# Kernel tuning notes

Hardware: AMD Instinct MI355X
Metric: run time of the kernel (lower is better)

The kernel has to match this reference:

```python
import jax, jax.numpy as jnp
import numpy as np

E = 1_000_000   # total edges across batch
B = 1024        # n_batch (graphs)
IN = 128
OUT = 128


def setup_inputs() -> dict:
    key = jax.random.key(0)
    ks = jax.random.split(key, 8)
    x1 = jax.random.normal(ks[0], (E, IN), dtype=jnp.float32)
    # cumulative slice boundaries: [0, sorted interior cuts, E]
    inner = jnp.sort(jax.random.randint(ks[1], (B - 1,), 0, E))
    edge_slices = jnp.concatenate([jnp.zeros((1,), jnp.int32),
                                   inner.astype(jnp.int32),
                                   jnp.full((1,), E, jnp.int32)])
    s1 = 1.0 / np.sqrt(IN)
    s2 = 1.0 / np.sqrt(OUT)
    W1 = jax.random.uniform(ks[2], (IN, OUT), jnp.float32, -s1, s1)
    b1 = jax.random.uniform(ks[3], (OUT,), jnp.float32, -s1, s1)
    W2 = jax.random.uniform(ks[4], (OUT, OUT), jnp.float32, -s2, s2)
    b2 = jax.random.uniform(ks[5], (OUT,), jnp.float32, -s2, s2)
    W3 = jax.random.uniform(ks[6], (OUT, OUT), jnp.float32, -s2, s2)
    b3 = jax.random.uniform(ks[7], (OUT,), jnp.float32, -s2, s2)
    return {"x1": x1, "edge_slices": edge_slices,
            "W1": W1, "b1": b1, "W2": W2, "b2": b2, "W3": W3, "b3": b3}


def reference(x1, edge_slices, W1, b1, W2, b2, W3, b3):
    n_edges = x1.shape[0]
    n_batch = edge_slices.shape[0] - 1
    # internal MLP: Linear -> ReLU -> Linear
    h = jax.nn.relu(x1 @ W1 + b1) @ W2 + b2  # [E, OUT]
    # segment id of edge i: index of slice containing i (replaces repeat_interleave)
    seg = jnp.searchsorted(edge_slices[1:], jnp.arange(n_edges), side='right')
    sums = jax.ops.segment_sum(h, seg, num_segments=n_batch)        # [B, OUT]
    counts = (edge_slices[1:] - edge_slices[:-1]).astype(h.dtype)   # [B]
    mean = sums / jnp.maximum(counts, 1.0)[:, None]  # empty segments -> 0 (matches scatter-mean)
    # external MLP: single Linear
    return mean @ W3 + b3
```

## Files before the change

### kernel.cpp

```cpp
#include <hip/hip_runtime.h>
#include <hip/hip_bf16.h>

typedef __attribute__((ext_vector_type(8))) short short8;
typedef __attribute__((ext_vector_type(4))) float floatx4;
typedef unsigned short u16;
typedef unsigned int u32;

#define D 128
#define TM 64
#define NT 4
#define CHUNK (TM*NT)
#define LDSX 136

static __device__ __forceinline__ u16 f2bf(float f) {
  union { float f; u32 u; } v; v.f = f;
  u32 r = v.u + 0x7fffu + ((v.u >> 16) & 1u);
  return (u16)(r >> 16);
}

__global__ void prep_kernel(const float* __restrict__ W1, u16* __restrict__ W1T,
                            float* __restrict__ S, int nS)
{
  int t = blockIdx.x * blockDim.x + threadIdx.x;
  if (t < D * D) {
    int k = t >> 7;
    int n = t & (D - 1);
    W1T[n * D + k] = f2bf(W1[t]);
  }
  if (t < nS) S[t] = 0.f;
}

__global__ __launch_bounds__(256, 3)
void fused_mlp_segsum(const float* __restrict__ x1,
                      const int* __restrict__ slices,
                      const u16* __restrict__ W1T,
                      const float* __restrict__ b1,
                      float* __restrict__ S,
                      int E, int B)
{
  __shared__ __align__(16) u16 xt[2][TM * LDSX];

  const int tid  = threadIdx.x;
  const int wv   = tid >> 6;
  const int lane = tid & 63;
  const int quad = lane >> 4;
  const int l16  = lane & 15;

  const int chunkStart = blockIdx.x * CHUNK;
  const int chunkEnd   = min(chunkStart + CHUNK, E);
  const int ntiles     = (chunkEnd - chunkStart + TM - 1) / TM;

  short8 bf[2][4];
  #pragma unroll
  for (int c = 0; c < 2; ++c)
    #pragma unroll
    for (int kk = 0; kk < 4; ++kk)
      bf[c][kk] = *(const short8*)(W1T + ((2 * wv + c) * 16 + l16) * D + kk * 32 + quad * 8);

  float bias[2] = { b1[wv * 32 + l16], b1[wv * 32 + 16 + l16] };

  int l = 0, r = B + 1;
  while (l < r) { int m = (l + r) >> 1; if (slices[m] <= chunkStart) l = m + 1; else r = m; }
  int cur = l - 1;
  float racc0 = 0.f, racc1 = 0.f;

  {
    #pragma unroll
    for (int i = 0; i < 8; ++i) {
      int f = tid + i * 256;
      int row = chunkStart + (f >> 5);
      int c = (f & 31) * 4;
      int rr = min(row, E - 1);
      float4 v = *(const float4*)(x1 + (size_t)rr * D + c);
      if (row >= E) { v.x = 0.f; v.y = 0.f; v.z = 0.f; v.w = 0.f; }
      uint2 pk;
      pk.x = (u32)f2bf(v.x) | ((u32)f2bf(v.y) << 16);
      pk.y = (u32)f2bf(v.z) | ((u32)f2bf(v.w) << 16);
      *(uint2*)(&xt[0][(f >> 5) * LDSX + c]) = pk;
    }
  }
  __syncthreads();

  for (int t = 0; t < ntiles; ++t) {
    const int base = chunkStart + t * TM;

    float4 ld[8];
    const bool havePf = (t + 1 < ntiles);
    if (havePf) {
      int nb = base + TM;
      #pragma unroll
      for (int i = 0; i < 8; ++i) {
        int f = tid + i * 256;
        int row = nb + (f >> 5);
        int rr = min(row, E - 1);
        ld[i] = *(const float4*)(x1 + (size_t)rr * D + (f & 31) * 4);
        if (row >= E) { ld[i].x = 0.f; ld[i].y = 0.f; ld[i].z = 0.f; ld[i].w = 0.f; }
      }
    }

    const u16* xb = xt[t & 1];
    floatx4 acc[4][2];
    #pragma unroll
    for (int rt = 0; rt < 4; ++rt)
      #pragma unroll
      for (int c = 0; c < 2; ++c)
        acc[rt][c] = (floatx4){0.f, 0.f, 0.f, 0.f};

    #pragma unroll
    for (int kk = 0; kk < 4; ++kk) {
      #pragma unroll
      for (int rt = 0; rt < 4; ++rt) {
        short8 a = *(const short8*)(xb + (rt * 16 + l16) * LDSX + kk * 32 + quad * 8);
        acc[rt][0] = __builtin_amdgcn_mfma_f32_16x16x32_bf16(a, bf[0][kk], acc[rt][0], 0, 0, 0);
        acc[rt][1] = __builtin_amdgcn_mfma_f32_16x16x32_bf16(a, bf[1][kk], acc[rt][1], 0, 0, 0);
      }
    }

    #pragma unroll
    for (int rt = 0; rt < 4; ++rt)
      #pragma unroll
      for (int c = 0; c < 2; ++c)
        #pragma unroll
        for (int i = 0; i < 4; ++i)
          acc[rt][c][i] = fmaxf(acc[rt][c][i] + bias[c], 0.f);

    const int tileHi = min(base + TM, chunkEnd);

    auto segAdd = [&](int loR, int hiR) {
      #pragma unroll
      for (int rt = 0; rt < 4; ++rt)
        #pragma unroll
        for (int i = 0; i < 4; ++i) {
          int rowOff = rt * 16 + quad * 4 + i;
          bool in = (rowOff >= loR) && (rowOff < hiR);
          racc0 += in ? acc[rt][0][i] : 0.f;
          racc1 += in ? acc[rt][1][i] : 0.f;
        }
    };
    auto flushSeg = [&](int s) {
      float t0 = racc0, t1 = racc1;
      t0 += __shfl_xor(t0, 16); t0 += __shfl_xor(t0, 32);
      t1 += __shfl_xor(t1, 16); t1 += __shfl_xor(t1, 32);
      if (quad == 0) {
        atomicAdd(&S[s * D + wv * 32 + l16], t0);
        atomicAdd(&S[s * D + wv * 32 + 16 + l16], t1);
      }
    };

    while (cur < B) {
      int segEnd = slices[cur + 1];
      if (segEnd > tileHi) break;
      int lo = max(slices[cur], base);
      if (segEnd > lo) segAdd(lo - base, segEnd - base);
      flushSeg(cur);
      racc0 = 0.f; racc1 = 0.f;
      ++cur;
    }
    if (cur < B) {
      int lo = max(slices[cur], base);
      if (lo < tileHi) {
        if (lo == base && tileHi == base + TM) {
          #pragma unroll
          for (int rt = 0; rt < 4; ++rt)
            #pragma unroll
            for (int i = 0; i < 4; ++i) { racc0 += acc[rt][0][i]; racc1 += acc[rt][1][i]; }
        } else {
          segAdd(lo - base, tileHi - base);
        }
      }
    }

    if (havePf) {
      u16* dst = xt[(t + 1) & 1];
      #pragma unroll
      for (int i = 0; i < 8; ++i) {
        int f = tid + i * 256;
        uint2 pk;
        pk.x = (u32)f2bf(ld[i].x) | ((u32)f2bf(ld[i].y) << 16);
        pk.y = (u32)f2bf(ld[i].z) | ((u32)f2bf(ld[i].w) << 16);
        *(uint2*)(&dst[(f >> 5) * LDSX + (f & 31) * 4]) = pk;
      }
    }
    __syncthreads();
  }

  if (cur < B && slices[cur] < chunkEnd) {
    float t0 = racc0, t1 = racc1;
    t0 += __shfl_xor(t0, 16); t0 += __shfl_xor(t0, 32);
    t1 += __shfl_xor(t1, 16); t1 += __shfl_xor(t1, 32);
    if (quad == 0) {
      atomicAdd(&S[cur * D + wv * 32 + l16], t0);
      atomicAdd(&S[cur * D + wv * 32 + 16 + l16], t1);
    }
  }
}

__global__ __launch_bounds__(128)
void finish_mlp(const float* __restrict__ S, const int* __restrict__ slices,
                const float* __restrict__ W2, const float* __restrict__ b2,
                const float* __restrict__ W3, const float* __restrict__ b3,
                float* __restrict__ out, int B)
{
  __shared__ float v0[D];
  __shared__ float v1[D];
  int s = blockIdx.x;
  int j = threadIdx.x;
  int c0 = slices[s], c1 = slices[s + 1];
  int cnt = c1 - c0;
  if (cnt <= 0) { out[s * D + j] = b3[j]; return; }
  v0[j] = S[s * D + j] * (1.f / (float)cnt);
  __syncthreads();
  float a = b2[j];
  #pragma unroll 8
  for (int k = 0; k < D; ++k) a = fmaf(v0[k], W2[k * D + j], a);
  v1[j] = a;
  __syncthreads();
  float o = b3[j];
  #pragma unroll 8
  for (int k = 0; k < D; ++k) o = fmaf(v1[k], W3[k * D + j], o);
  out[s * D + j] = o;
}

extern "C" void kernel_launch(void* const* d_in, const int* in_sizes, int n_in,
                              void* d_out, int out_size, void* d_ws, size_t ws_size,
                              hipStream_t stream) {
  const float* x1     = (const float*)d_in[0];
  const int*   slices = (const int*)d_in[1];
  const float* W1     = (const float*)d_in[2];
  const float* b1     = (const float*)d_in[3];
  const float* W2     = (const float*)d_in[4];
  const float* b2     = (const float*)d_in[5];
  const float* W3     = (const float*)d_in[6];
  const float* b3     = (const float*)d_in[7];
  float* out = (float*)d_out;

  const int E = in_sizes[0] / D;
  const int B = in_sizes[1] - 1;

  float* S   = (float*)d_ws;
  u16*   W1T = (u16*)((char*)d_ws + (size_t)B * D * 4);

  int nS = B * D;
  prep_kernel<<<(nS + 255) / 256, 256, 0, stream>>>(W1, W1T, S, nS);

  int nblk = (E + CHUNK - 1) / CHUNK;
  fused_mlp_segsum<<<nblk, 256, 0, stream>>>(x1, slices, W1T, b1, S, E, B);

  finish_mlp<<<B, D, 0, stream>>>(S, slices, W2, b2, W3, b3, out, B);
}
```

Before: 675.8 us.

## Stage x1 tiles into LDS via direct global-to-LDS loads with swizzle

```diff
diff --git a/kernel.cpp b/kernel.cpp
--- a/kernel.cpp
+++ b/kernel.cpp
@@ -7,16 +7,23 @@
 typedef unsigned int u32;
 
 #define D 128
-#define TM 64
-#define NT 4
+#define TM 32
+#define NT 8
 #define CHUNK (TM*NT)
-#define LDSX 136
 
 static __device__ __forceinline__ u16 f2bf(float f) {
   union { float f; u32 u; } v; v.f = f;
   u32 r = v.u + 0x7fffu + ((v.u >> 16) & 1u);
   return (u16)(r >> 16);
 }
+
+static __device__ __forceinline__ u32 pk2(float x, float y) {
+  union { __hip_bfloat162 h; u32 u; } c;
+  c.h = __float22bfloat162_rn(make_float2(x, y));
+  return c.u;
+}
+
+union S8u { short8 s; u32 u[4]; };
 
 __global__ void prep_kernel(const float* __restrict__ W1, u16* __restrict__ W1T,
                             float* __restrict__ S, int nS)
@@ -30,7 +37,7 @@
   if (t < nS) S[t] = 0.f;
 }
 
-__global__ __launch_bounds__(256, 3)
+__global__ __launch_bounds__(256, 4)
 void fused_mlp_segsum(const float* __restrict__ x1,
                       const int* __restrict__ slices,
                       const u16* __restrict__ W1T,
@@ -38,7 +45,7 @@
                       float* __restrict__ S,
                       int E, int B)
 {
-  __shared__ __align__(16) u16 xt[2][TM * LDSX];
+  __shared__ __align__(16) float xt[2][TM * D];
 
   const int tid  = threadIdx.x;
   const int wv   = tid >> 6;
@@ -59,49 +66,45 @@
 
   float bias[2] = { b1[wv * 32 + l16], b1[wv * 32 + 16 + l16] };
 
+  const int idxA = l16 * D + ((( quad * 2     ) ^ (l16 & 7)) << 2);
+  const int idxB = l16 * D + (((quad * 2 + 1) ^ (l16 & 7)) << 2);
+
+  const int pg  = lane & 31;
+  const int rhi = lane >> 5;
+
+  auto stage = [&](float* buf, int rowBase) {
+    #pragma unroll
+    for (int i = 0; i < 4; ++i) {
+      int rs = wv * 8 + i * 2 + rhi;
+      int lg = (pg & 24) | ((pg ^ rs) & 7);
+      int grow = min(rowBase + rs, E - 1);
+      const float* src = x1 + (size_t)grow * D + lg * 4;
+      float* dst = buf + rs * D + pg * 4;
+      __builtin_amdgcn_global_load_lds(
+          (const __attribute__((address_space(1))) void*)src,
+          (__attribute__((address_space(3))) void*)dst, 16, 0, 0);
+    }
+  };
+
   int l = 0, r = B + 1;
   while (l < r) { int m = (l + r) >> 1; if (slices[m] <= chunkStart) l = m + 1; else r = m; }
   int cur = l - 1;
+  int curStart = slices[cur];
+  int nextEnd  = slices[cur + 1];
   float racc0 = 0.f, racc1 = 0.f;
 
-  {
-    #pragma unroll
-    for (int i = 0; i < 8; ++i) {
-      int f = tid + i * 256;
-      int row = chunkStart + (f >> 5);
-      int c = (f & 31) * 4;
-      int rr = min(row, E - 1);
-      float4 v = *(const float4*)(x1 + (size_t)rr * D + c);
-      if (row >= E) { v.x = 0.f; v.y = 0.f; v.z = 0.f; v.w = 0.f; }
-      uint2 pk;
-      pk.x = (u32)f2bf(v.x) | ((u32)f2bf(v.y) << 16);
-      pk.y = (u32)f2bf(v.z) | ((u32)f2bf(v.w) << 16);
-      *(uint2*)(&xt[0][(f >> 5) * LDSX + c]) = pk;
-    }
-  }
+  stage(xt[0], chunkStart);
   __syncthreads();
 
   for (int t = 0; t < ntiles; ++t) {
     const int base = chunkStart + t * TM;
 
-    float4 ld[8];
-    const bool havePf = (t + 1 < ntiles);
-    if (havePf) {
-      int nb = base + TM;
-      #pragma unroll
-      for (int i = 0; i < 8; ++i) {
-        int f = tid + i * 256;
-        int row = nb + (f >> 5);
-        int rr = min(row, E - 1);
-        ld[i] = *(const float4*)(x1 + (size_t)rr * D + (f & 31) * 4);
-        if (row >= E) { ld[i].x = 0.f; ld[i].y = 0.f; ld[i].z = 0.f; ld[i].w = 0.f; }
-      }
-    }
-
-    const u16* xb = xt[t & 1];
-    floatx4 acc[4][2];
-    #pragma unroll
-    for (int rt = 0; rt < 4; ++rt)
+    if (t + 1 < ntiles) stage(xt[(t + 1) & 1], base + TM);
+
+    const float* xb = xt[t & 1];
+    floatx4 acc[2][2];
+    #pragma unroll
+    for (int rt = 0; rt < 2; ++rt)
       #pragma unroll
       for (int c = 0; c < 2; ++c)
         acc[rt][c] = (floatx4){0.f, 0.f, 0.f, 0.f};
@@ -109,15 +112,19 @@
     #pragma unroll
     for (int kk = 0; kk < 4; ++kk) {
       #pragma unroll
-      for (int rt = 0; rt < 4; ++rt) {
-        short8 a = *(const short8*)(xb + (rt * 16 + l16) * LDSX + kk * 32 + quad * 8);
-        acc[rt][0] = __builtin_amdgcn_mfma_f32_16x16x32_bf16(a, bf[0][kk], acc[rt][0], 0, 0, 0);
-        acc[rt][1] = __builtin_amdgcn_mfma_f32_16x16x32_bf16(a, bf[1][kk], acc[rt][1], 0, 0, 0);
+      for (int rt = 0; rt < 2; ++rt) {
+        float4 fa = *(const float4*)(xb + idxA + rt * 2048 + kk * 32);
+        float4 fb = *(const float4*)(xb + idxB + rt * 2048 + kk * 32);
+        S8u a;
+        a.u[0] = pk2(fa.x, fa.y); a.u[1] = pk2(fa.z, fa.w);
+        a.u[2] = pk2(fb.x, fb.y); a.u[3] = pk2(fb.z, fb.w);
+        acc[rt][0] = __builtin_amdgcn_mfma_f32_16x16x32_bf16(a.s, bf[0][kk], acc[rt][0], 0, 0, 0);
+        acc[rt][1] = __builtin_amdgcn_mfma_f32_16x16x32_bf16(a.s, bf[1][kk], acc[rt][1], 0, 0, 0);
       }
     }
 
     #pragma unroll
-    for (int rt = 0; rt < 4; ++rt)
+    for (int rt = 0; rt < 2; ++rt)
       #pragma unroll
       for (int c = 0; c < 2; ++c)
         #pragma unroll
@@ -128,7 +135,7 @@
 
     auto segAdd = [&](int loR, int hiR) {
       #pragma unroll
-      for (int rt = 0; rt < 4; ++rt)
+      for (int rt = 0; rt < 2; ++rt)
         #pragma unroll
         for (int i = 0; i < 4; ++i) {
           int rowOff = rt * 16 + quad * 4 + i;
@@ -147,21 +154,21 @@
       }
     };
 
-    while (cur < B) {
-      int segEnd = slices[cur + 1];
-      if (segEnd > tileHi) break;
-      int lo = max(slices[cur], base);
-      if (segEnd > lo) segAdd(lo - base, segEnd - base);
+    while (nextEnd <= tileHi) {
+      int lo = max(curStart, base);
+      if (nextEnd > lo) segAdd(lo - base, nextEnd - base);
       flushSeg(cur);
       racc0 = 0.f; racc1 = 0.f;
+      curStart = nextEnd;
       ++cur;
-    }
-    if (cur < B) {
-      int lo = max(slices[cur], base);
+      nextEnd = (cur < B) ? slices[cur + 1] : 0x7fffffff;
+    }
+    {
+      int lo = max(curStart, base);
       if (lo < tileHi) {
         if (lo == base && tileHi == base + TM) {
           #pragma unroll
-          for (int rt = 0; rt < 4; ++rt)
+          for (int rt = 0; rt < 2; ++rt)
             #pragma unroll
             for (int i = 0; i < 4; ++i) { racc0 += acc[rt][0][i]; racc1 += acc[rt][1][i]; }
         } else {
@@ -170,21 +177,10 @@
       }
     }
 
-    if (havePf) {
-      u16* dst = xt[(t + 1) & 1];
-      #pragma unroll
-      for (int i = 0; i < 8; ++i) {
-        int f = tid + i * 256;
-        uint2 pk;
-        pk.x = (u32)f2bf(ld[i].x) | ((u32)f2bf(ld[i].y) << 16);
-        pk.y = (u32)f2bf(ld[i].z) | ((u32)f2bf(ld[i].w) << 16);
-        *(uint2*)(&dst[(f >> 5) * LDSX + (f & 31) * 4]) = pk;
-      }
-    }
     __syncthreads();
   }
 
-  if (cur < B && slices[cur] < chunkEnd) {
+  if (cur < B && curStart < chunkEnd) {
     float t0 = racc0, t1 = racc1;
     t0 += __shfl_xor(t0, 16); t0 += __shfl_xor(t0, 32);
     t1 += __shfl_xor(t1, 16); t1 += __shfl_xor(t1, 32);
```

Result: no change. 679.1 us (+0.5%).
